# Optimization experiments

Hardware: AMD Instinct MI355X
Metric: run time of the kernel (lower is better)

The kernel has to match this reference:

```python
import jax, jax.numpy as jnp
import numpy as np

N = 6000      # num_nodes
NS = 4500     # observed subset size
B = 8         # batch
D = 192       # embedding_dim = 128 + 64
GDIM = 40     # node_dim for graph constructor
K = 10        # graph_k (top-k neighbors)
L = 3         # num_recon_graph_layers
ALPHA = 3.0   # graph constructor alpha


def setup_inputs() -> dict:
    key = jax.random.key(0)
    ks = jax.random.split(key, 12)
    def rn(k, shape, s=0.05):
        return jax.random.normal(k, shape, jnp.float32) * s
    return {
        "subset_embedding": jax.random.normal(ks[0], (B, NS, D), jnp.float32),
        "idx_subset": jax.random.randint(ks[1], (NS,), 0, N),
        "emb1": rn(ks[2], (N, GDIM), 1.0),
        "emb2": rn(ks[3], (N, GDIM), 1.0),
        "lin1_w": rn(ks[4], (GDIM, GDIM)), "lin1_b": jnp.zeros((GDIM,), jnp.float32),
        "lin2_w": rn(ks[5], (GDIM, GDIM)), "lin2_b": jnp.zeros((GDIM,), jnp.float32),
        "unobserved_init": rn(ks[6], (1, 1, D), 0.01),
        "mlp_w": rn(ks[7], (L, D, D)), "mlp_b": jnp.zeros((L, D), jnp.float32),
        "gate_w": rn(ks[8], (L, 2 * D, D)), "gate_b": jnp.zeros((L, D), jnp.float32),
        "diff_w": rn(ks[9], (L, 2 * D, D)), "diff_b": jnp.zeros((L, D), jnp.float32),
        "confidence_alpha": jnp.float32(0.3),
    }


def _build_adj(emb1, emb2, l1w, l1b, l2w, l2b):
    # ImprovedGraphConstructor (eval mode: hard top-k mask)
    nv1 = jnp.tanh(ALPHA * (emb1 @ l1w + l1b))          # (N, GDIM)
    nv2 = jnp.tanh(ALPHA * (emb2 @ l2w + l2b))
    a = nv1 @ nv2.T                                      # (N, N)
    adj = 0.5 * (a + a.T)
    adj = jax.nn.softplus(adj) - 0.5
    _, idx = jax.lax.top_k(adj, K)                       # (N, K) per-row top-k
    mask = jnp.zeros_like(adj).at[jnp.arange(N)[:, None], idx].set(1.0)
    return jax.nn.relu(adj * mask)


def _norm_adj(adj):
    # symmetric normalization D^(-1/2) (A + I) D^(-1/2)
    adj = adj + jnp.eye(N, dtype=adj.dtype)
    d = adj.sum(1)
    d_safe = jnp.where(d > 0, d, 1.0)
    dis = jnp.where(d > 0, jax.lax.rsqrt(d_safe), 0.0)
    return adj * dis[:, None] * dis[None, :]


def reference(subset_embedding, idx_subset, emb1, emb2, lin1_w, lin1_b,
              lin2_w, lin2_b, unobserved_init, mlp_w, mlp_b,
              gate_w, gate_b, diff_w, diff_b, confidence_alpha):
    adj = _build_adj(emb1, emb2, lin1_w, lin1_b, lin2_w, lin2_b)
    norm_adj = _norm_adj(adj)

    # preprocess_embedding: scatter observed embeddings into learned init
    h0 = jnp.broadcast_to(unobserved_init, (B, N, D)).at[:, idx_subset, :].set(subset_embedding)
    conf = jnp.zeros((B, N, 1), jnp.float32).at[:, idx_subset, :].set(1.0)

    h = h0
    for i in range(L):
        # ImprovedGraphConvLayer (dropout = identity at eval)
        agg = jnp.einsum('bnc,nm->bmc', h, norm_adj)     # (B, N, D)
        hn = agg @ mlp_w[i] + mlp_b[i]
        g = jax.nn.sigmoid(jnp.concatenate([h, hn], axis=-1) @ gate_w[i] + gate_b[i])
        layer_out = g * hn + (1.0 - g) * h               # highway
        # learnable diffusion gate fusing layer output with previous state
        dg = jax.nn.sigmoid(jnp.concatenate([h, layer_out], axis=-1) @ diff_w[i] + diff_b[i])
        h = dg * layer_out + (1.0 - dg) * h

    # confidence-based fusion: observed nodes keep mostly their original embedding
    return conf * ((1.0 - confidence_alpha) * h0 + confidence_alpha * h) + (1.0 - conf) * h
```

## Files before the change

### kernel.cpp

```cpp
#include <hip/hip_runtime.h>
#include <math.h>

#define NN 6000
#define NSUB 4500
#define BB 8
#define DD 192
#define GD 40
#define KTOP 10
#define NLAY 3
#define ROWS (BB*NN)
#define NEDGE (NN*(KTOP+1))
#define WMAT (DD*DD)
#define NSTRIP 8
#define SCOLS 750
#define NTILE 12
#define RCAP 6016
#define SP 100

typedef unsigned short u16;
typedef unsigned int u32;
typedef __attribute__((ext_vector_type(8))) short bf16x8;
typedef __attribute__((ext_vector_type(8))) _Float16 f16x8;
typedef __attribute__((ext_vector_type(4))) float f32x4;

__device__ __forceinline__ u16 f2b(float x){
  u32 u = __float_as_uint(x);
  u32 r = (u + 0x7fffu + ((u >> 16) & 1u)) >> 16;
  return (u16)r;
}
__device__ __forceinline__ float b2f(u16 h){
  u32 u = ((u32)h) << 16; return __uint_as_float(u);
}
__device__ __forceinline__ u32 fkey(float f){
  u32 b = __float_as_uint(f);
  return (b & 0x80000000u) ? ~b : (b | 0x80000000u);
}
__device__ __forceinline__ u32 packh2(float a, float b){
  _Float16 ha = (_Float16)a, hb = (_Float16)b;
  u16 ua = __builtin_bit_cast(u16, ha), ub = __builtin_bit_cast(u16, hb);
  return (u32)ua | ((u32)ub << 16);
}
__device__ __forceinline__ u32 packl2(float a, float b){
  _Float16 ha = (_Float16)a, hb = (_Float16)b;
  _Float16 la = (_Float16)(a - (float)ha), lb = (_Float16)(b - (float)hb);
  u16 ua = __builtin_bit_cast(u16, la), ub = __builtin_bit_cast(u16, lb);
  return (u32)ua | ((u32)ub << 16);
}
__device__ __forceinline__ f16x8 ldfrag(const u16* p){
  union { f16x8 v; double d[2]; } u;
  const double* q = (const double*)p;
  u.d[0] = q[0]; u.d[1] = q[1];
  return u.v;
}

__global__ void k_prep_uv(const float* __restrict__ emb1, const float* __restrict__ emb2,
                          const float* __restrict__ w1, const float* __restrict__ b1,
                          const float* __restrict__ w2, const float* __restrict__ b2,
                          float* __restrict__ U, float* __restrict__ V){
  int id = blockIdx.x*blockDim.x + threadIdx.x;
  if (id >= NN*GD) return;
  int i = id / GD, g = id % GD;
  float s1 = b1[g], s2 = b2[g];
  for (int k = 0; k < GD; k++){
    s1 += emb1[i*GD+k]*w1[k*GD+g];
    s2 += emb2[i*GD+k]*w2[k*GD+g];
  }
  float n1 = tanhf(3.0f*s1), n2 = tanhf(3.0f*s2);
  U[i*80+g]    = 0.5f*n1;  U[i*80+40+g] = 0.5f*n2;
  V[i*80+g]    = n2;       V[i*80+40+g] = n1;
}

__global__ __launch_bounds__(256, 3) void k_scoretopk(const float* __restrict__ U, const float* __restrict__ V,
                          float* __restrict__ ptv, int* __restrict__ ptc){
  __shared__ u32 Uarr[64*SP];
  __shared__ u32 Varr[64*SP];
  __shared__ u32 rowthr[64];
  u16* Uh = (u16*)Uarr;  u16* Ul = Uh + 64*SP;
  u16* Vh = (u16*)Varr;  u16* Vl = Vh + 64*SP;

  const int tid = threadIdx.x, lane = tid & 63, wave = tid >> 6;
  const int q = lane >> 4, ln = lane & 15;
  const int r0 = blockIdx.x*64;
  const int y  = blockIdx.y;
  const int cstart = y*SCOLS, cend = cstart + SCOLS;
  const float NINF = -__builtin_inff();
  const int lrow = wave*16 + ln;

  for (int idx = tid; idx < 64*24; idx += 256){
    int r = idx & 63, c4 = idx >> 6;
    float4 u = {0.f,0.f,0.f,0.f};
    if (c4 < 20){
      int gr = r0 + r; if (gr > NN-1) gr = NN-1;
      u = *(const float4*)&U[(size_t)gr*80 + c4*4];
    }
    Uarr[r*50 + c4*2    ] = packh2(u.x, u.y);
    Uarr[r*50 + c4*2 + 1] = packh2(u.z, u.w);
    ((u32*)Ul)[r*50 + c4*2    ] = packl2(u.x, u.y);
    ((u32*)Ul)[r*50 + c4*2 + 1] = packl2(u.z, u.w);
  }
  if (tid < 64) rowthr[tid] = 0u;
  __syncthreads();

  f16x8 Uhf[3], Ulf[3];
  #pragma unroll
  for (int ks = 0; ks < 3; ks++){
    Uhf[ks] = ldfrag(&Uh[lrow*SP + ks*32 + q*8]);
    Ulf[ks] = ldfrag(&Ul[lrow*SP + ks*32 + q*8]);
  }

  float tv[10]; int ti[10];
  #pragma unroll
  for (int s = 0; s < 10; s++){ tv[s] = NINF; ti[s] = NN; }

  for (int t = 0; t < NTILE; t++){
    int cb = cstart + t*64;
    __syncthreads();
    for (int idx = tid; idx < 64*24; idx += 256){
      int r = idx & 63, c4 = idx >> 6;
      float4 v = {0.f,0.f,0.f,0.f};
      if (c4 < 20){
        int gc = cb + r; if (gc > NN-1) gc = NN-1;
        v = *(const float4*)&V[(size_t)gc*80 + c4*4];
      }
      Varr[r*50 + c4*2    ] = packh2(v.x, v.y);
      Varr[r*50 + c4*2 + 1] = packh2(v.z, v.w);
      ((u32*)Vl)[r*50 + c4*2    ] = packl2(v.x, v.y);
      ((u32*)Vl)[r*50 + c4*2 + 1] = packl2(v.z, v.w);
    }
    __syncthreads();

    f32x4 acc[4];
    #pragma unroll
    for (int ch = 0; ch < 4; ch++) acc[ch] = (f32x4){0.f,0.f,0.f,0.f};
    #pragma unroll
    for (int ks = 0; ks < 3; ks++){
      #pragma unroll
      for (int ch = 0; ch < 4; ch++){
        f16x8 vh = ldfrag(&Vh[(ch*16 + ln)*SP + ks*32 + q*8]);
        f16x8 vl = ldfrag(&Vl[(ch*16 + ln)*SP + ks*32 + q*8]);
        acc[ch] = __builtin_amdgcn_mfma_f32_16x16x32_f16(vh, Uhf[ks], acc[ch], 0, 0, 0);
        acc[ch] = __builtin_amdgcn_mfma_f32_16x16x32_f16(vh, Ulf[ks], acc[ch], 0, 0, 0);
        acc[ch] = __builtin_amdgcn_mfma_f32_16x16x32_f16(vl, Uhf[ks], acc[ch], 0, 0, 0);
      }
    }

    u32 Treg = rowthr[lrow];
    #pragma unroll
    for (int ch = 0; ch < 4; ch++){
      #pragma unroll
      for (int rg = 0; rg < 4; rg++){
        int j = cb + ch*16 + q*4 + rg;
        float v = acc[ch][rg];
        u32 uk = fkey(v);
        if (j < cend && uk > Treg && v > tv[9]){
          bool b[9];
          #pragma unroll
          for (int k = 0; k < 9; k++) b[k] = v > tv[k];
          #pragma unroll
          for (int k = 9; k >= 1; k--){
            bool bh = b[k-1];
            bool bk = (k == 9) ? true : b[k];
            tv[k] = bh ? tv[k-1] : (bk ? v : tv[k]);
            ti[k] = bh ? ti[k-1] : (bk ? j : ti[k]);
          }
          if (b[0]){ tv[0] = v; ti[0] = j; }
          u32 k9 = fkey(tv[9]);
          if (k9 > Treg) Treg = k9;
          atomicMax(&rowthr[lrow], k9);
        }
      }
    }
  }

  __syncthreads();
  float* candv = (float*)Uarr;
  int*   candi = (int*)(Uarr + 64*41);
  #pragma unroll
  for (int s = 0; s < 10; s++){
    candv[lrow*41 + q*10 + s] = tv[s];
    candi[lrow*41 + q*10 + s] = ti[s];
  }
  __syncthreads();
  if (tid < 64 && r0 + tid < NN){
    int row = tid;
    u32 P = 0;
    for (int s = 0; s < 10; s++){
      float bv = NINF; int bi = NN; int by = 0;
      #pragma unroll
      for (int g = 0; g < 4; g++){
        u32 pg = (P >> (8*g)) & 255u;
        u32 pc = pg < 9u ? pg : 9u;
        float v = candv[row*41 + g*10 + pc];
        int  jj = candi[row*41 + g*10 + pc];
        if (pg >= 10u){ v = NINF; jj = NN; }
        if (v > bv || (v == bv && jj < bi)){ bv = v; bi = jj; by = g; }
      }
      P += (1u << (8*by));
      size_t o = ((size_t)y*RCAP + r0 + row)*10 + s;
      ptv[o] = bv; ptc[o] = bi;
    }
  }
}

__global__ void k_mergetopk(const float* __restrict__ ptv, const int* __restrict__ ptc,
                            int* __restrict__ topcols, float* __restrict__ topvals,
                            float* __restrict__ dis){
  int r = blockIdx.x*blockDim.x + threadIdx.x;
  if (r >= NN) return;
  const float NINF = -__builtin_inff();
  unsigned long long P = 0;
  float d = 1.0f;
  for (int s = 0; s < 10; s++){
    float bv = NINF; int bi = NN; int by = 0;
    #pragma unroll
    for (int g = 0; g < 8; g++){
      u32 pg = (u32)((P >> (8*g)) & 255u);
      u32 pc = pg < 9u ? pg : 9u;
      size_t o = ((size_t)g*RCAP + r)*10 + pc;
      float v = ptv[o]; int jj = ptc[o];
      if (pg >= 10u){ v = NINF; jj = NN; }
      if (v > bv || (v == bv && jj < bi)){ bv = v; bi = jj; by = g; }
    }
    P += (1ull << (8*by));
    float sp = (bv > 20.f) ? bv : log1pf(expf(bv));
    float a = sp - 0.5f; if (a < 0.f) a = 0.f;
    topvals[r*KTOP + s] = a; topcols[r*KTOP + s] = bi;
    d += a;
  }
  dis[r] = rsqrtf(d);
}

__global__ void k_count(const int* __restrict__ topcols, int* __restrict__ counts){
  int id = blockIdx.x*blockDim.x + threadIdx.x;
  if (id >= NEDGE) return;
  int n = id / (KTOP+1), e = id % (KTOP+1);
  int m = (e < KTOP) ? topcols[n*KTOP+e] : n;
  atomicAdd(&counts[m], 1);
}

__global__ __launch_bounds__(1024) void k_scan(const int* __restrict__ counts,
                                               int* __restrict__ rowptr, int* __restrict__ cursor){
  __shared__ int part[1024];
  int t = threadIdx.x;
  int local[6];
  int s = 0, base = t*6;
  for (int q = 0; q < 6; q++){
    int i = base + q; int c = (i < NN) ? counts[i] : 0;
    local[q] = s; s += c;
  }
  part[t] = s; __syncthreads();
  for (int off = 1; off < 1024; off <<= 1){
    int v = (t >= off) ? part[t-off] : 0;
    __syncthreads();
    part[t] += v;
    __syncthreads();
  }
  int excl = (t > 0) ? part[t-1] : 0;
  for (int q = 0; q < 6; q++){
    int i = base + q;
    if (i < NN){ int p = excl + local[q]; rowptr[i] = p; cursor[i] = p; }
  }
  if (t == 1023) rowptr[NN] = part[1023];
}

__global__ void k_fill(const int* __restrict__ topcols, const float* __restrict__ topvals,
                       const float* __restrict__ dis, int* __restrict__ cursor,
                       int* __restrict__ csr_src, float* __restrict__ csr_w){
  int id = blockIdx.x*blockDim.x + threadIdx.x;
  if (id >= NEDGE) return;
  int n = id / (KTOP+1), e = id % (KTOP+1);
  int m; float v;
  if (e < KTOP){ m = topcols[n*KTOP+e]; v = topvals[n*KTOP+e]; }
  else { m = n; v = 1.0f; }
  float w = v * dis[n] * dis[m];
  int pos = atomicAdd(&cursor[m], 1);
  csr_src[pos] = n; csr_w[pos] = w;
}

__global__ void k_winner(const int* __restrict__ idx, int* __restrict__ winner){
  int s = blockIdx.x*blockDim.x + threadIdx.x;
  if (s >= NSUB) return;
  atomicMax(&winner[idx[s]], s);
}

__global__ void k_h0(const float* __restrict__ subset, const float* __restrict__ uinit,
                     const int* __restrict__ winner, u16* __restrict__ h){
  int id = blockIdx.x*blockDim.x + threadIdx.x;
  if (id >= ROWS*DD) return;
  int c = id % DD; int bn = id / DD; int n = bn % NN; int b = bn / NN;
  int w = winner[n];
  float v = (w >= 0) ? subset[((size_t)b*NSUB + w)*DD + c] : uinit[c];
  h[id] = f2b(v);
}

__global__ void k_wprep(const float* __restrict__ mlp_w, const float* __restrict__ gate_w,
                        const float* __restrict__ diff_w, u16* __restrict__ wbf){
  int id = blockIdx.x*blockDim.x + threadIdx.x;
  if (id >= NLAY*5*WMAT) return;
  int mat = id / WMAT, rem = id % WMAT;
  int n = rem / DD, k = rem % DD;
  int layer = mat / 5, which = mat % 5;
  float v;
  if (which == 0)      v = mlp_w [((size_t)layer*DD   + k      )*DD + n];
  else if (which == 1) v = gate_w[((size_t)layer*2*DD + k      )*DD + n];
  else if (which == 2) v = gate_w[((size_t)layer*2*DD + DD + k )*DD + n];
  else if (which == 3) v = diff_w[((size_t)layer*2*DD + k      )*DD + n];
  else                 v = diff_w[((size_t)layer*2*DD + DD + k )*DD + n];
  wbf[id] = f2b(v);
}

__global__ __launch_bounds__(192) void k_spmm(const u16* __restrict__ h, const int* __restrict__ rowptr,
                       const int* __restrict__ csr_src, const float* __restrict__ csr_w,
                       u16* __restrict__ agg){
  __shared__ int s_src[256]; __shared__ float s_w[256];
  int m = blockIdx.x; int c = threadIdx.x;
  int beg = rowptr[m], end = rowptr[m+1];
  float acc[BB];
  #pragma unroll
  for (int b = 0; b < BB; b++) acc[b] = 0.f;
  for (int base = beg; base < end; base += 256){
    int cnt = end - base; if (cnt > 256) cnt = 256;
    __syncthreads();
    for (int e = threadIdx.x; e < cnt; e += 192){ s_src[e] = csr_src[base+e]; s_w[e] = csr_w[base+e]; }
    __syncthreads();
    for (int e = 0; e < cnt; e++){
      int src = s_src[e]; float w = s_w[e];
      const u16* hp = h + (size_t)src*DD + c;
      #pragma unroll
      for (int b = 0; b < BB; b++) acc[b] += w * b2f(hp[(size_t)b*NN*DD]);
    }
  }
  #pragma unroll
  for (int b = 0; b < BB; b++) agg[((size_t)b*NN + m)*DD + c] = f2b(acc[b]);
}

#define LP 200
__global__ __launch_bounds__(256, 2) void k_layer(u16* __restrict__ h, const u16* __restrict__ agg,
                        const u16* __restrict__ wl, const float* __restrict__ mb,
                        const float* __restrict__ gb, const float* __restrict__ db){
  __shared__ u16 Ah[64*LP];
  __shared__ u16 Ax[64*LP];
  const int tid = threadIdx.x, lane = tid & 63, wave = tid >> 6;
  const int q = lane >> 4, ln = lane & 15;
  const int row0 = blockIdx.x*64;

  for (int i = tid; i < 64*24; i += 256){
    int r = i/24, c0 = i%24;
    ((uint4*)&Ah[r*LP])[c0] = ((const uint4*)h  )[(size_t)(row0+r)*24 + c0];
    ((uint4*)&Ax[r*LP])[c0] = ((const uint4*)agg)[(size_t)(row0+r)*24 + c0];
  }
  __syncthreads();

  const u16 *Wm = wl, *G1 = wl + WMAT, *G2 = wl + 2*WMAT, *D1 = wl + 3*WMAT, *D2 = wl + 4*WMAT;

  f32x4 acc[4][3];
  bf16x8 Bf[6][3];

  auto loadB = [&](const u16* wp){
    #pragma unroll
    for (int kk = 0; kk < 6; kk++)
      #pragma unroll
      for (int ntl = 0; ntl < 3; ntl++){
        int nt = wave*3 + ntl;
        Bf[kk][ntl] = *(const bf16x8*)&wp[(size_t)(nt*16 + ln)*DD + kk*32 + q*8];
      }
  };
  auto gemm = [&](const u16* Al){
    #pragma unroll
    for (int kk = 0; kk < 6; kk++){
      bf16x8 a[4];
      #pragma unroll
      for (int rt = 0; rt < 4; rt++)
        a[rt] = *(const bf16x8*)&Al[(rt*16 + ln)*LP + kk*32 + q*8];
      #pragma unroll
      for (int rt = 0; rt < 4; rt++)
        #pragma unroll
        for (int ntl = 0; ntl < 3; ntl++)
          acc[rt][ntl] = __builtin_amdgcn_mfma_f32_16x16x32_bf16(a[rt], Bf[kk][ntl], acc[rt][ntl], 0, 0, 0);
    }
  };
  auto zacc = [&](){
    #pragma unroll
    for (int rt = 0; rt < 4; rt++)
      #pragma unroll
      for (int ntl = 0; ntl < 3; ntl++)
        acc[rt][ntl] = (f32x4){0.f, 0.f, 0.f, 0.f};
  };

  zacc(); loadB(Wm); gemm(Ax);
  __syncthreads();
  #pragma unroll
  for (int ntl = 0; ntl < 3; ntl++){
    int col = (wave*3 + ntl)*16 + ln; float bias = mb[col];
    #pragma unroll
    for (int rt = 0; rt < 4; rt++)
      #pragma unroll
      for (int r = 0; r < 4; r++)
        Ax[(rt*16 + q*4 + r)*LP + col] = f2b(acc[rt][ntl][r] + bias);
  }
  __syncthreads();

  zacc(); loadB(G1); gemm(Ah); loadB(G2); gemm(Ax);
  __syncthreads();
  #pragma unroll
  for (int ntl = 0; ntl < 3; ntl++){
    int col = (wave*3 + ntl)*16 + ln; float bias = gb[col];
    #pragma unroll
    for (int rt = 0; rt < 4; rt++)
      #pragma unroll
      for (int r = 0; r < 4; r++){
        int off = (rt*16 + q*4 + r)*LP + col;
        float g = 1.f/(1.f + expf(-(acc[rt][ntl][r] + bias)));
        float hv = b2f(Ah[off]), hnv = b2f(Ax[off]);
        Ax[off] = f2b(g*hnv + (1.f - g)*hv);
      }
  }
  __syncthreads();

  zacc(); loadB(D1); gemm(Ah); loadB(D2); gemm(Ax);
  #pragma unroll
  for (int ntl = 0; ntl < 3; ntl++){
    int col = (wave*3 + ntl)*16 + ln; float bias = db[col];
    #pragma unroll
    for (int rt = 0; rt < 4; rt++)
      #pragma unroll
      for (int r = 0; r < 4; r++){
        int row = rt*16 + q*4 + r; int off = row*LP + col;
        float dg = 1.f/(1.f + expf(-(acc[rt][ntl][r] + bias)));
        float lov = b2f(Ax[off]), hv = b2f(Ah[off]);
        h[(size_t)(row0 + row)*DD + col] = f2b(dg*lov + (1.f - dg)*hv);
      }
  }
}

__global__ void k_final(const u16* __restrict__ h, const float* __restrict__ subset,
                        const int* __restrict__ winner, const float* __restrict__ ca_p,
                        float* __restrict__ out){
  int id = blockIdx.x*blockDim.x + threadIdx.x;
  if (id >= ROWS*DD) return;
  int c = id % DD; int bn = id / DD; int n = bn % NN; int b = bn / NN;
  float ca = ca_p[0];
  int w = winner[n];
  float hv = b2f(h[id]);
  float o;
  if (w >= 0){
    float h0 = subset[((size_t)b*NSUB + w)*DD + c];
    o = (1.0f - ca)*h0 + ca*hv;
  } else {
    o = hv;
  }
  out[id] = o;
}

extern "C" void kernel_launch(void* const* d_in, const int* in_sizes, int n_in,
                              void* d_out, int out_size, void* d_ws, size_t ws_size,
                              hipStream_t stream) {
  const float* subset = (const float*)d_in[0];
  const int*   idxs   = (const int*)  d_in[1];
  const float* emb1   = (const float*)d_in[2];
  const float* emb2   = (const float*)d_in[3];
  const float* l1w    = (const float*)d_in[4];
  const float* l1b    = (const float*)d_in[5];
  const float* l2w    = (const float*)d_in[6];
  const float* l2b    = (const float*)d_in[7];
  const float* uinit  = (const float*)d_in[8];
  const float* mlp_w  = (const float*)d_in[9];
  const float* mlp_b  = (const float*)d_in[10];
  const float* gate_w = (const float*)d_in[11];
  const float* gate_b = (const float*)d_in[12];
  const float* diff_w = (const float*)d_in[13];
  const float* diff_b = (const float*)d_in[14];
  const float* ca     = (const float*)d_in[15];
  float* out = (float*)d_out;

  char* base = (char*)d_ws; size_t off = 0;
  auto alloc = [&](size_t b)->void*{ void* p = base + off; off += b; off = (off + 255) & ~(size_t)255; return p; };
  float* U       = (float*)alloc((size_t)NN*80*4);
  float* V       = (float*)alloc((size_t)NN*80*4);
  u16*   h       = (u16*)  alloc((size_t)ROWS*DD*2);
  u16*   agg     = (u16*)  alloc((size_t)ROWS*DD*2);
  u16*   wbf     = (u16*)  alloc((size_t)NLAY*5*WMAT*2);
  int*   topcols = (int*)  alloc((size_t)NN*KTOP*4);
  float* topvals = (float*)alloc((size_t)NN*KTOP*4);
  float* dis     = (float*)alloc((size_t)NN*4);
  int*   winner  = (int*)  alloc((size_t)NN*4);
  int*   counts  = (int*)  alloc((size_t)NN*4);
  int*   rowptr  = (int*)  alloc((size_t)(NN+1)*4);
  int*   cursor  = (int*)  alloc((size_t)NN*4);
  int*   csr_src = (int*)  alloc((size_t)NEDGE*4);
  float* csr_w   = (float*)alloc((size_t)NEDGE*4);
  float* ptv     = (float*)alloc((size_t)NSTRIP*RCAP*KTOP*4);
  int*   ptc     = (int*)  alloc((size_t)NSTRIP*RCAP*KTOP*4);

  k_prep_uv<<<(NN*GD + 255)/256, 256, 0, stream>>>(emb1, emb2, l1w, l1b, l2w, l2b, U, V);

  dim3 gs(94, NSTRIP);
  k_scoretopk<<<gs, 256, 0, stream>>>(U, V, ptv, ptc);
  k_mergetopk<<<(NN + 255)/256, 256, 0, stream>>>(ptv, ptc, topcols, topvals, dis);

  hipMemsetAsync(counts, 0, (size_t)NN*4, stream);
  k_count<<<(NEDGE + 255)/256, 256, 0, stream>>>(topcols, counts);
  k_scan<<<1, 1024, 0, stream>>>(counts, rowptr, cursor);
  k_fill<<<(NEDGE + 255)/256, 256, 0, stream>>>(topcols, topvals, dis, cursor, csr_src, csr_w);

  hipMemsetAsync(winner, 0xFF, (size_t)NN*4, stream);
  k_winner<<<(NSUB + 255)/256, 256, 0, stream>>>(idxs, winner);
  k_h0<<<(ROWS*DD + 255)/256, 256, 0, stream>>>(subset, uinit, winner, h);

  k_wprep<<<(NLAY*5*WMAT + 255)/256, 256, 0, stream>>>(mlp_w, gate_w, diff_w, wbf);

  for (int l = 0; l < NLAY; l++){
    k_spmm<<<NN, 192, 0, stream>>>(h, rowptr, csr_src, csr_w, agg);
    k_layer<<<ROWS/64, 256, 0, stream>>>(h, agg, wbf + (size_t)l*5*WMAT,
                                         mlp_b + l*DD, gate_b + l*DD, diff_b + l*DD);
  }

  k_final<<<(ROWS*DD + 255)/256, 256, 0, stream>>>(h, subset, winner, ca, out);
}
```

Measured before the change: 554.0 us.

## Precompute fp16 hi/lo split, vectorize spmm/h0/final, early-skip topk candidates

Several independent changes land together. The fp16 hi/lo split of U and V now happens once in the prep kernel, so the score kernel only does wide uint4 copies into shared memory instead of converting on every tile. The top-k insertion first checks the max of each 4-value group so groups below the threshold are skipped. SpMM now has each thread handle 8 channels of one batch with 16-byte loads, and h0 and the final kernel work on pairs of elements. Bounds guards on column indices were added to count and fill, and the prep buffers use more global memory.

```diff
diff --git a/kernel.cpp b/kernel.cpp
--- a/kernel.cpp
+++ b/kernel.cpp
@@ -15,7 +15,8 @@
 #define SCOLS 750
 #define NTILE 12
 #define RCAP 6016
-#define SP 100
+#define KP 96
+#define SP2 104
 
 typedef unsigned short u16;
 typedef unsigned int u32;
@@ -35,16 +36,11 @@
   u32 b = __float_as_uint(f);
   return (b & 0x80000000u) ? ~b : (b | 0x80000000u);
 }
-__device__ __forceinline__ u32 packh2(float a, float b){
-  _Float16 ha = (_Float16)a, hb = (_Float16)b;
-  u16 ua = __builtin_bit_cast(u16, ha), ub = __builtin_bit_cast(u16, hb);
-  return (u32)ua | ((u32)ub << 16);
-}
-__device__ __forceinline__ u32 packl2(float a, float b){
-  _Float16 ha = (_Float16)a, hb = (_Float16)b;
-  _Float16 la = (_Float16)(a - (float)ha), lb = (_Float16)(b - (float)hb);
-  u16 ua = __builtin_bit_cast(u16, la), ub = __builtin_bit_cast(u16, lb);
-  return (u32)ua | ((u32)ub << 16);
+__device__ __forceinline__ void wr_hl(u16* __restrict__ H, u16* __restrict__ L, size_t off, float x){
+  _Float16 hx = (_Float16)x;
+  H[off] = __builtin_bit_cast(u16, hx);
+  _Float16 lx = (_Float16)(x - (float)hx);
+  L[off] = __builtin_bit_cast(u16, lx);
 }
 __device__ __forceinline__ f16x8 ldfrag(const u16* p){
   union { f16x8 v; double d[2]; } u;
@@ -56,7 +52,8 @@
 __global__ void k_prep_uv(const float* __restrict__ emb1, const float* __restrict__ emb2,
                           const float* __restrict__ w1, const float* __restrict__ b1,
                           const float* __restrict__ w2, const float* __restrict__ b2,
-                          float* __restrict__ U, float* __restrict__ V){
+                          u16* __restrict__ Uh, u16* __restrict__ Ul,
+                          u16* __restrict__ Vh, u16* __restrict__ Vl){
   int id = blockIdx.x*blockDim.x + threadIdx.x;
   if (id >= NN*GD) return;
   int i = id / GD, g = id % GD;
@@ -66,17 +63,26 @@
     s2 += emb2[i*GD+k]*w2[k*GD+g];
   }
   float n1 = tanhf(3.0f*s1), n2 = tanhf(3.0f*s2);
-  U[i*80+g]    = 0.5f*n1;  U[i*80+40+g] = 0.5f*n2;
-  V[i*80+g]    = n2;       V[i*80+40+g] = n1;
-}
-
-__global__ __launch_bounds__(256, 3) void k_scoretopk(const float* __restrict__ U, const float* __restrict__ V,
+  size_t base = (size_t)i*KP;
+  wr_hl(Uh, Ul, base + g,      0.5f*n1);
+  wr_hl(Uh, Ul, base + 40 + g, 0.5f*n2);
+  wr_hl(Vh, Vl, base + g,      n2);
+  wr_hl(Vh, Vl, base + 40 + g, n1);
+  if (g < 16){
+    Uh[base+80+g] = 0; Ul[base+80+g] = 0;
+    Vh[base+80+g] = 0; Vl[base+80+g] = 0;
+  }
+}
+
+__global__ __launch_bounds__(256, 3) void k_scoretopk(
+                          const u16* __restrict__ Uh, const u16* __restrict__ Ul,
+                          const u16* __restrict__ Vh, const u16* __restrict__ Vl,
                           float* __restrict__ ptv, int* __restrict__ ptc){
-  __shared__ u32 Uarr[64*SP];
-  __shared__ u32 Varr[64*SP];
+  __shared__ u16 Us[2*64*SP2];
+  __shared__ u16 Vs[2*64*SP2];
   __shared__ u32 rowthr[64];
-  u16* Uh = (u16*)Uarr;  u16* Ul = Uh + 64*SP;
-  u16* Vh = (u16*)Varr;  u16* Vl = Vh + 64*SP;
+  u16* Ushi = Us;        u16* Uslo = Us + 64*SP2;
+  u16* Vshi = Vs;        u16* Vslo = Vs + 64*SP2;
 
   const int tid = threadIdx.x, lane = tid & 63, wave = tid >> 6;
   const int q = lane >> 4, ln = lane & 15;
@@ -86,17 +92,11 @@
   const float NINF = -__builtin_inff();
   const int lrow = wave*16 + ln;
 
-  for (int idx = tid; idx < 64*24; idx += 256){
-    int r = idx & 63, c4 = idx >> 6;
-    float4 u = {0.f,0.f,0.f,0.f};
-    if (c4 < 20){
-      int gr = r0 + r; if (gr > NN-1) gr = NN-1;
-      u = *(const float4*)&U[(size_t)gr*80 + c4*4];
-    }
-    Uarr[r*50 + c4*2    ] = packh2(u.x, u.y);
-    Uarr[r*50 + c4*2 + 1] = packh2(u.z, u.w);
-    ((u32*)Ul)[r*50 + c4*2    ] = packl2(u.x, u.y);
-    ((u32*)Ul)[r*50 + c4*2 + 1] = packl2(u.z, u.w);
+  for (int idx = tid; idx < 64*12; idx += 256){
+    int r = idx/12, c4 = idx%12;
+    int gr = r0 + r; if (gr > NN-1) gr = NN-1;
+    *(uint4*)&Ushi[r*SP2 + c4*8] = *(const uint4*)&Uh[(size_t)gr*KP + c4*8];
+    *(uint4*)&Uslo[r*SP2 + c4*8] = *(const uint4*)&Ul[(size_t)gr*KP + c4*8];
   }
   if (tid < 64) rowthr[tid] = 0u;
   __syncthreads();
@@ -104,8 +104,8 @@
   f16x8 Uhf[3], Ulf[3];
   #pragma unroll
   for (int ks = 0; ks < 3; ks++){
-    Uhf[ks] = ldfrag(&Uh[lrow*SP + ks*32 + q*8]);
-    Ulf[ks] = ldfrag(&Ul[lrow*SP + ks*32 + q*8]);
+    Uhf[ks] = ldfrag(&Ushi[lrow*SP2 + ks*32 + q*8]);
+    Ulf[ks] = ldfrag(&Uslo[lrow*SP2 + ks*32 + q*8]);
   }
 
   float tv[10]; int ti[10];
@@ -115,17 +115,11 @@
   for (int t = 0; t < NTILE; t++){
     int cb = cstart + t*64;
     __syncthreads();
-    for (int idx = tid; idx < 64*24; idx += 256){
-      int r = idx & 63, c4 = idx >> 6;
-      float4 v = {0.f,0.f,0.f,0.f};
-      if (c4 < 20){
-        int gc = cb + r; if (gc > NN-1) gc = NN-1;
-        v = *(const float4*)&V[(size_t)gc*80 + c4*4];
-      }
-      Varr[r*50 + c4*2    ] = packh2(v.x, v.y);
-      Varr[r*50 + c4*2 + 1] = packh2(v.z, v.w);
-      ((u32*)Vl)[r*50 + c4*2    ] = packl2(v.x, v.y);
-      ((u32*)Vl)[r*50 + c4*2 + 1] = packl2(v.z, v.w);
+    for (int idx = tid; idx < 64*12; idx += 256){
+      int r = idx/12, c4 = idx%12;
+      int gc = cb + r; if (gc > NN-1) gc = NN-1;
+      *(uint4*)&Vshi[r*SP2 + c4*8] = *(const uint4*)&Vh[(size_t)gc*KP + c4*8];
+      *(uint4*)&Vslo[r*SP2 + c4*8] = *(const uint4*)&Vl[(size_t)gc*KP + c4*8];
     }
     __syncthreads();
 
@@ -136,8 +130,8 @@
     for (int ks = 0; ks < 3; ks++){
       #pragma unroll
       for (int ch = 0; ch < 4; ch++){
-        f16x8 vh = ldfrag(&Vh[(ch*16 + ln)*SP + ks*32 + q*8]);
-        f16x8 vl = ldfrag(&Vl[(ch*16 + ln)*SP + ks*32 + q*8]);
+        f16x8 vh = ldfrag(&Vshi[(ch*16 + ln)*SP2 + ks*32 + q*8]);
+        f16x8 vl = ldfrag(&Vslo[(ch*16 + ln)*SP2 + ks*32 + q*8]);
         acc[ch] = __builtin_amdgcn_mfma_f32_16x16x32_f16(vh, Uhf[ks], acc[ch], 0, 0, 0);
         acc[ch] = __builtin_amdgcn_mfma_f32_16x16x32_f16(vh, Ulf[ks], acc[ch], 0, 0, 0);
         acc[ch] = __builtin_amdgcn_mfma_f32_16x16x32_f16(vl, Uhf[ks], acc[ch], 0, 0, 0);
@@ -147,34 +141,37 @@
     u32 Treg = rowthr[lrow];
     #pragma unroll
     for (int ch = 0; ch < 4; ch++){
-      #pragma unroll
-      for (int rg = 0; rg < 4; rg++){
-        int j = cb + ch*16 + q*4 + rg;
-        float v = acc[ch][rg];
-        u32 uk = fkey(v);
-        if (j < cend && uk > Treg && v > tv[9]){
-          bool b[9];
-          #pragma unroll
-          for (int k = 0; k < 9; k++) b[k] = v > tv[k];
-          #pragma unroll
-          for (int k = 9; k >= 1; k--){
-            bool bh = b[k-1];
-            bool bk = (k == 9) ? true : b[k];
-            tv[k] = bh ? tv[k-1] : (bk ? v : tv[k]);
-            ti[k] = bh ? ti[k-1] : (bk ? j : ti[k]);
+      float mm = fmaxf(fmaxf(acc[ch][0], acc[ch][1]), fmaxf(acc[ch][2], acc[ch][3]));
+      if (mm > tv[9] && fkey(mm) > Treg){
+        #pragma unroll
+        for (int rg = 0; rg < 4; rg++){
+          int j = cb + ch*16 + q*4 + rg;
+          float v = acc[ch][rg];
+          u32 uk = fkey(v);
+          if (j < cend && uk > Treg && v > tv[9]){
+            bool b[9];
+            #pragma unroll
+            for (int k = 0; k < 9; k++) b[k] = v > tv[k];
+            #pragma unroll
+            for (int k = 9; k >= 1; k--){
+              bool bh = b[k-1];
+              bool bk = (k == 9) ? true : b[k];
+              tv[k] = bh ? tv[k-1] : (bk ? v : tv[k]);
+              ti[k] = bh ? ti[k-1] : (bk ? j : ti[k]);
+            }
+            if (b[0]){ tv[0] = v; ti[0] = j; }
+            u32 k9 = fkey(tv[9]);
+            if (k9 > Treg) Treg = k9;
+            atomicMax(&rowthr[lrow], k9);
           }
-          if (b[0]){ tv[0] = v; ti[0] = j; }
-          u32 k9 = fkey(tv[9]);
-          if (k9 > Treg) Treg = k9;
-          atomicMax(&rowthr[lrow], k9);
         }
       }
     }
   }
 
   __syncthreads();
-  float* candv = (float*)Uarr;
-  int*   candi = (int*)(Uarr + 64*41);
+  float* candv = (float*)Us;
+  int*   candi = (int*)((u32*)Us + 64*41);
   #pragma unroll
   for (int s = 0; s < 10; s++){
     candv[lrow*41 + q*10 + s] = tv[s];
@@ -235,6 +232,7 @@
   if (id >= NEDGE) return;
   int n = id / (KTOP+1), e = id % (KTOP+1);
   int m = (e < KTOP) ? topcols[n*KTOP+e] : n;
+  if ((unsigned)m >= NN) m = n;
   atomicAdd(&counts[m], 1);
 }
 
@@ -272,6 +270,7 @@
   int m; float v;
   if (e < KTOP){ m = topcols[n*KTOP+e]; v = topvals[n*KTOP+e]; }
   else { m = n; v = 1.0f; }
+  if ((unsigned)m >= NN){ m = n; v = 0.0f; }
   float w = v * dis[n] * dis[m];
   int pos = atomicAdd(&cursor[m], 1);
   csr_src[pos] = n; csr_w[pos] = w;
@@ -286,11 +285,13 @@
 __global__ void k_h0(const float* __restrict__ subset, const float* __restrict__ uinit,
                      const int* __restrict__ winner, u16* __restrict__ h){
   int id = blockIdx.x*blockDim.x + threadIdx.x;
-  if (id >= ROWS*DD) return;
-  int c = id % DD; int bn = id / DD; int n = bn % NN; int b = bn / NN;
+  if (id >= ROWS*(DD/2)) return;
+  int c2 = id % (DD/2); int bn = id / (DD/2); int n = bn % NN; int b = bn / NN;
   int w = winner[n];
-  float v = (w >= 0) ? subset[((size_t)b*NSUB + w)*DD + c] : uinit[c];
-  h[id] = f2b(v);
+  float2 v;
+  if (w >= 0) v = *(const float2*)&subset[((size_t)b*NSUB + w)*DD + c2*2];
+  else        v = *(const float2*)&uinit[c2*2];
+  ((u32*)h)[id] = (u32)f2b(v.x) | ((u32)f2b(v.y) << 16);
 }
 
 __global__ void k_wprep(const float* __restrict__ mlp_w, const float* __restrict__ gate_w,
@@ -312,26 +313,37 @@
 __global__ __launch_bounds__(192) void k_spmm(const u16* __restrict__ h, const int* __restrict__ rowptr,
                        const int* __restrict__ csr_src, const float* __restrict__ csr_w,
                        u16* __restrict__ agg){
-  __shared__ int s_src[256]; __shared__ float s_w[256];
-  int m = blockIdx.x; int c = threadIdx.x;
+  __shared__ int s_src[128]; __shared__ float s_w[128];
+  int m = blockIdx.x;
+  int c8 = threadIdx.x % 24;
+  int b  = threadIdx.x / 24;
   int beg = rowptr[m], end = rowptr[m+1];
-  float acc[BB];
-  #pragma unroll
-  for (int b = 0; b < BB; b++) acc[b] = 0.f;
-  for (int base = beg; base < end; base += 256){
-    int cnt = end - base; if (cnt > 256) cnt = 256;
+  float acc[8];
+  #pragma unroll
+  for (int i = 0; i < 8; i++) acc[i] = 0.f;
+  for (int base = beg; base < end; base += 128){
+    int cnt = end - base; if (cnt > 128) cnt = 128;
     __syncthreads();
     for (int e = threadIdx.x; e < cnt; e += 192){ s_src[e] = csr_src[base+e]; s_w[e] = csr_w[base+e]; }
     __syncthreads();
     for (int e = 0; e < cnt; e++){
       int src = s_src[e]; float w = s_w[e];
-      const u16* hp = h + (size_t)src*DD + c;
-      #pragma unroll
-      for (int b = 0; b < BB; b++) acc[b] += w * b2f(hp[(size_t)b*NN*DD]);
-    }
-  }
-  #pragma unroll
-  for (int b = 0; b < BB; b++) agg[((size_t)b*NN + m)*DD + c] = f2b(acc[b]);
+      uint4 pk = *(const uint4*)&h[((size_t)b*NN + src)*DD + c8*8];
+      u32 ws[4] = {pk.x, pk.y, pk.z, pk.w};
+      #pragma unroll
+      for (int t2 = 0; t2 < 4; t2++){
+        u32 u = ws[t2];
+        acc[t2*2]   += w * __uint_as_float(u << 16);
+        acc[t2*2+1] += w * __uint_as_float(u & 0xffff0000u);
+      }
+    }
+  }
+  uint4 o;
+  o.x = (u32)f2b(acc[0]) | ((u32)f2b(acc[1]) << 16);
+  o.y = (u32)f2b(acc[2]) | ((u32)f2b(acc[3]) << 16);
+  o.z = (u32)f2b(acc[4]) | ((u32)f2b(acc[5]) << 16);
+  o.w = (u32)f2b(acc[6]) | ((u32)f2b(acc[7]) << 16);
+  *(uint4*)&agg[((size_t)b*NN + m)*DD + c8*8] = o;
 }
 
 #define LP 200
@@ -437,19 +449,22 @@
                         const int* __restrict__ winner, const float* __restrict__ ca_p,
                         float* __restrict__ out){
   int id = blockIdx.x*blockDim.x + threadIdx.x;
-  if (id >= ROWS*DD) return;
-  int c = id % DD; int bn = id / DD; int n = bn % NN; int b = bn / NN;
+  if (id >= ROWS*(DD/2)) return;
+  int c2 = id % (DD/2); int bn = id / (DD/2); int n = bn % NN; int b = bn / NN;
   float ca = ca_p[0];
   int w = winner[n];
-  float hv = b2f(h[id]);
-  float o;
+  u32 hp = ((const u32*)h)[id];
+  float hlo = __uint_as_float(hp << 16);
+  float hhi = __uint_as_float(hp & 0xffff0000u);
+  float2 o;
   if (w >= 0){
-    float h0 = subset[((size_t)b*NSUB + w)*DD + c];
-    o = (1.0f - ca)*h0 + ca*hv;
+    float2 h0 = *(const float2*)&subset[((size_t)b*NSUB + w)*DD + c2*2];
+    o.x = (1.0f - ca)*h0.x + ca*hlo;
+    o.y = (1.0f - ca)*h0.y + ca*hhi;
   } else {
-    o = hv;
-  }
-  out[id] = o;
+    o.x = hlo; o.y = hhi;
+  }
+  *(float2*)&out[(size_t)bn*DD + c2*2] = o;
 }
 
 extern "C" void kernel_launch(void* const* d_in, const int* in_sizes, int n_in,
@@ -475,8 +490,10 @@
 
   char* base = (char*)d_ws; size_t off = 0;
   auto alloc = [&](size_t b)->void*{ void* p = base + off; off += b; off = (off + 255) & ~(size_t)255; return p; };
-  float* U       = (float*)alloc((size_t)NN*80*4);
-  float* V       = (float*)alloc((size_t)NN*80*4);
+  u16*   Uht     = (u16*)  alloc((size_t)NN*KP*2);
+  u16*   Ult     = (u16*)  alloc((size_t)NN*KP*2);
+  u16*   Vht     = (u16*)  alloc((size_t)NN*KP*2);
+  u16*   Vlt     = (u16*)  alloc((size_t)NN*KP*2);
   u16*   h       = (u16*)  alloc((size_t)ROWS*DD*2);
   u16*   agg     = (u16*)  alloc((size_t)ROWS*DD*2);
   u16*   wbf     = (u16*)  alloc((size_t)NLAY*5*WMAT*2);
@@ -492,10 +509,11 @@
   float* ptv     = (float*)alloc((size_t)NSTRIP*RCAP*KTOP*4);
   int*   ptc     = (int*)  alloc((size_t)NSTRIP*RCAP*KTOP*4);
 
-  k_prep_uv<<<(NN*GD + 255)/256, 256, 0, stream>>>(emb1, emb2, l1w, l1b, l2w, l2b, U, V);
+  k_prep_uv<<<(NN*GD + 255)/256, 256, 0, stream>>>(emb1, emb2, l1w, l1b, l2w, l2b,
+                                                   Uht, Ult, Vht, Vlt);
 
   dim3 gs(94, NSTRIP);
-  k_scoretopk<<<gs, 256, 0, stream>>>(U, V, ptv, ptc);
+  k_scoretopk<<<gs, 256, 0, stream>>>(Uht, Ult, Vht, Vlt, ptv, ptc);
   k_mergetopk<<<(NN + 255)/256, 256, 0, stream>>>(ptv, ptc, topcols, topvals, dis);
 
   hipMemsetAsync(counts, 0, (size_t)NN*4, stream);
@@ -505,7 +523,7 @@
 
   hipMemsetAsync(winner, 0xFF, (size_t)NN*4, stream);
   k_winner<<<(NSUB + 255)/256, 256, 0, stream>>>(idxs, winner);
-  k_h0<<<(ROWS*DD + 255)/256, 256, 0, stream>>>(subset, uinit, winner, h);
+  k_h0<<<(ROWS*(DD/2) + 255)/256, 256, 0, stream>>>(subset, uinit, winner, h);
 
   k_wprep<<<(NLAY*5*WMAT + 255)/256, 256, 0, stream>>>(mlp_w, gate_w, diff_w, wbf);
 
@@ -515,5 +533,5 @@
                                          mlp_b + l*DD, gate_b + l*DD, diff_b + l*DD);
   }
 
-  k_final<<<(ROWS*DD + 255)/256, 256, 0, stream>>>(h, subset, winner, ca, out);
-}
+  k_final<<<(ROWS*(DD/2) + 255)/256, 256, 0, stream>>>(h, subset, winner, ca, out);
+}
```

Result: faster. 505.8 us (-8.7%).
